# Kernel optimization log

Hardware: AMD Instinct MI355X
Metric: run time of the kernel (lower is better)

The kernel has to match this reference:

```python
import jax, jax.numpy as jnp
import numpy as np

INPUT_SIZE = 1
HIDDEN = 50
OUTPUT = 1
BATCH = 2048
SEQ = 512


def _lstm_layer(x, W_ih, W_hh, b_ih, b_hh):
    # x: [B, T, I]; W_ih: [4H, I]; W_hh: [4H, H]; biases: [4H]
    B = x.shape[0]
    H = W_hh.shape[1]
    # Precompute input contributions for all timesteps: [B, T, 4H]
    xg = jnp.einsum('bti,gi->btg', x, W_ih) + b_ih + b_hh

    def step(carry, xg_t):
        h, c = carry                      # [B, H] each
        g = xg_t + h @ W_hh.T             # [B, 4H]
        i, f, gg, o = jnp.split(g, 4, axis=-1)  # PyTorch gate order i,f,g,o
        i = jax.nn.sigmoid(i)
        f = jax.nn.sigmoid(f)
        gg = jnp.tanh(gg)
        o = jax.nn.sigmoid(o)
        c = f * c + i * gg
        h = o * jnp.tanh(c)
        return (h, c), h

    h0 = jnp.zeros((B, H), x.dtype)
    c0 = jnp.zeros((B, H), x.dtype)
    _, hs = jax.lax.scan(step, (h0, c0), jnp.swapaxes(xg, 0, 1))  # hs: [T, B, H]
    return jnp.swapaxes(hs, 0, 1)  # [B, T, H]


def setup_inputs() -> dict:
    key = jax.random.key(0)
    ks = jax.random.split(key, 11)
    s = 1.0 / np.sqrt(HIDDEN)  # PyTorch LSTM init scale
    x = jax.random.normal(ks[0], (BATCH, SEQ, INPUT_SIZE), dtype=jnp.float32)
    W_ih0 = jax.random.uniform(ks[1], (4 * HIDDEN, INPUT_SIZE), minval=-s, maxval=s)
    W_hh0 = jax.random.uniform(ks[2], (4 * HIDDEN, HIDDEN), minval=-s, maxval=s)
    b_ih0 = jax.random.uniform(ks[3], (4 * HIDDEN,), minval=-s, maxval=s)
    b_hh0 = jax.random.uniform(ks[4], (4 * HIDDEN,), minval=-s, maxval=s)
    W_ih1 = jax.random.uniform(ks[5], (4 * HIDDEN, HIDDEN), minval=-s, maxval=s)
    W_hh1 = jax.random.uniform(ks[6], (4 * HIDDEN, HIDDEN), minval=-s, maxval=s)
    b_ih1 = jax.random.uniform(ks[7], (4 * HIDDEN,), minval=-s, maxval=s)
    b_hh1 = jax.random.uniform(ks[8], (4 * HIDDEN,), minval=-s, maxval=s)
    fc_W = jax.random.uniform(ks[9], (OUTPUT, HIDDEN), minval=-s, maxval=s)
    fc_b = jax.random.uniform(ks[10], (OUTPUT,), minval=-s, maxval=s)
    return {
        'x': x,
        'W_ih0': W_ih0, 'W_hh0': W_hh0, 'b_ih0': b_ih0, 'b_hh0': b_hh0,
        'W_ih1': W_ih1, 'W_hh1': W_hh1, 'b_ih1': b_ih1, 'b_hh1': b_hh1,
        'fc_W': fc_W, 'fc_b': fc_b,
    }


def reference(x, W_ih0, W_hh0, b_ih0, b_hh0, W_ih1, W_hh1, b_ih1, b_hh1, fc_W, fc_b):
    h1 = _lstm_layer(x, W_ih0, W_hh0, b_ih0, b_hh0)   # [B, T, H]
    h2 = _lstm_layer(h1, W_ih1, W_hh1, b_ih1, b_hh1)  # [B, T, H]
    last = h2[:, -1, :]                               # [B, H]
    return last @ fc_W.T + fc_b                       # [B, OUTPUT]
```

## Files before the change

### kernel.cpp

```cpp
#include <hip/hip_runtime.h>

typedef _Float16 f16x8 __attribute__((ext_vector_type(8)));
typedef float    f32x4 __attribute__((ext_vector_type(4)));

constexpr int BATCH = 2048;
constexpr int SEQ   = 512;
constexpr int H     = 50;
constexpr int NB    = 8;
constexpr int NT    = 832;
constexpr int KQ    = 4;
constexpr int PSZ   = 1024;

__device__ __forceinline__ float fexp2(float x) { return __builtin_amdgcn_exp2f(x); }
__device__ __forceinline__ float frcp(float x)  { return __builtin_amdgcn_rcpf(x); }
__device__ __forceinline__ _Float16 f16hi(float w) { return (_Float16)w; }
__device__ __forceinline__ _Float16 f16lo(float w) {
    _Float16 h = (_Float16)w; return (_Float16)(w - (float)h);
}
__device__ __forceinline__ int caddr(int k, int c) {
    return ((k >> 3) * 64) + c * 8 + (k & 7);
}
union H2U { unsigned u; _Float16 h[2]; };

constexpr float K1 = 1.4426950408889634f;
constexpr float K2 = 2.8853900817779268f;


__global__ __launch_bounds__(NT, 3) void lstm2_r17(
    const float* __restrict__ x,
    const float* __restrict__ Wih0, const float* __restrict__ Whh0,
    const float* __restrict__ bih0, const float* __restrict__ bhh0,
    const float* __restrict__ Wih1, const float* __restrict__ Whh1,
    const float* __restrict__ bih1, const float* __restrict__ bhh1,
    const float* __restrict__ fcW,  const float* __restrict__ fcb,
    float* __restrict__ out)
{
    __shared__ _Float16 sB[2][PSZ];
    __shared__ unsigned sXu[SEQ * NB];
    __shared__ float    sH2f[H * NB];

    const int t    = threadIdx.x;
    const int wave = t >> 6, lane = t & 63;
    const int quad = lane >> 4, nn = lane & 15;
    const int bbase = blockIdx.x * NB;

    for (int i = t; i < 2 * PSZ; i += NT) ((_Float16*)sB)[i] = (_Float16)0.f;

    for (int i = t; i < NB * SEQ; i += NT) {
        const int b = i >> 9, s = i & (SEQ - 1);
        const float xv = x[(bbase + b) * SEQ + s];
        H2U p; p.h[0] = f16hi(xv); p.h[1] = f16lo(xv);
        sXu[s * NB + b] = p.u;
    }

    const int  m    = wave;
    const int  jr   = m * 4 + (nn >> 2);
    const int  gate = nn & 3;
    const bool rv   = (jr < H);
    const int  lrow = gate * H + jr;
    const float rsc = (gate == 2) ? -K2 : -K1;

    f16x8 a0[2];
    f16x8 a1[KQ];
    #pragma unroll
    for (int q = 0; q < 2; ++q) {
        #pragma unroll
        for (int j = 0; j < 8; ++j) {
            const int k = q * 32 + quad * 8 + j;
            _Float16 v = (_Float16)0.f;
            if (rv) {
                if      (k < 50)   v = (_Float16)(rsc * Whh0[lrow * H + k]);
                else if (k == 50)  v = f16hi(rsc * Wih0[lrow]);
                else if (k == 51)  v = f16lo(rsc * Wih0[lrow]);
            }
            a0[q][j] = v;
        }
    }
    #pragma unroll
    for (int q = 0; q < KQ; ++q) {
        #pragma unroll
        for (int j = 0; j < 8; ++j) {
            const int k = q * 32 + quad * 8 + j;
            _Float16 v = (_Float16)0.f;
            if (rv) {
                if      (k < 50)              v = (_Float16)(rsc * Wih1[lrow * H + k]);
                else if (k >= 64 && k < 114)  v = (_Float16)(rsc * Whh1[lrow * H + (k - 64)]);
            }
            a1[q][j] = v;
        }
    }

    const int  hiH  = nn >> 3;
    const int  col  = nn & 7;
    const int  jj   = m * 4 + quad;
    const bool jv   = (jj < H);

    f32x4 b0v = {0,0,0,0}, b1v = {0,0,0,0};
    if (jv) {
        #pragma unroll
        for (int r = 0; r < 4; ++r) {
            const float s = (r == 2) ? -K2 : -K1;
            b0v[r] = s * (bih0[r * H + jj] + bhh0[r * H + jj]);
            b1v[r] = s * (bih1[r * H + jj] + bhh1[r * H + jj]);
        }
    }

    const int rb0 = 0 * 256 + quad * 64 + col * 8;
    const int rb1 = 1 * 256 + quad * 64 + col * 8;
    const int rb2 = 2 * 256 + quad * 64 + col * 8;
    const int rb3 = 3 * 256 + quad * 64 + col * 8;
    const int  wH   = caddr(hiH * 64 + jj, col);
    const bool wrOK = jv;
    float c = 0.f;

    const bool xstage = (wave == 12) && (quad == 2) && (hiH == 0);
    const int  xwr    = (384 + col * 8 + 2) >> 1;

    __syncthreads();
    if (t < NB)
        ((unsigned*)sB[0])[(384 + t * 8 + 2) >> 1] = sXu[t];
    __syncthreads();

    auto body = [&](int s, const _Float16* __restrict__ br,
                    _Float16* __restrict__ bw,
                    bool doL0, bool doL1, bool last) {
        const f16x8 bq0 = *(const f16x8*)&br[rb0];
        const f16x8 bq1 = *(const f16x8*)&br[rb1];
        const f16x8 bq2 = *(const f16x8*)&br[rb2];
        const f16x8 bq3 = *(const f16x8*)&br[rb3];

        f32x4 g0 = b0v;
        g0 = __builtin_amdgcn_mfma_f32_16x16x32_f16(a0[0], bq0, g0, 0, 0, 0);
        g0 = __builtin_amdgcn_mfma_f32_16x16x32_f16(a0[1], bq1, g0, 0, 0, 0);
        f32x4 g1a = b1v;
        g1a = __builtin_amdgcn_mfma_f32_16x16x32_f16(a1[0], bq0, g1a, 0, 0, 0);
        g1a = __builtin_amdgcn_mfma_f32_16x16x32_f16(a1[1], bq1, g1a, 0, 0, 0);
        f32x4 g1b = {0, 0, 0, 0};
        g1b = __builtin_amdgcn_mfma_f32_16x16x32_f16(a1[2], bq2, g1b, 0, 0, 0);
        g1b = __builtin_amdgcn_mfma_f32_16x16x32_f16(a1[3], bq3, g1b, 0, 0, 0);

        float g[4];
        #pragma unroll
        for (int r = 0; r < 4; ++r)
            g[r] = hiH ? (g1a[r] + g1b[r]) : g0[r];

        const bool act = hiH ? doL1 : doL0;
        if (act) {
            float Ei = fexp2(g[0]);
            float Ef = fexp2(g[1]);
            float Eg = fexp2(-fabsf(g[2]));
            float Eo = fexp2(g[3]);
            float P  = (1.f + Ei) * (1.f + Eg);
            float F  = 1.f + Ef;
            float R  = frcp(P * F);
            float tn = copysignf((1.f - Eg) * F, -g[2]);
            c = fmaf(c, P, tn) * R;
            float Ec = fexp2(-fabsf(K2 * c));
            float h  = copysignf((1.f - Ec) * frcp((1.f + Eo) * (1.f + Ec)), c);
            if (wrOK) {
                if (last && hiH) {
                    sH2f[jj * NB + col] = h;
                } else {
                    bw[wH] = (_Float16)h;
                }
            }
        }
        if (xstage)
            ((unsigned*)bw)[xwr] = sXu[((s + 1) & (SEQ - 1)) * NB + col];
        __syncthreads();
    };

    body(0, sB[0], sB[1], true, false, false);
    #pragma unroll 1
    for (int i = 0; i < 255; ++i) {
        body(2 * i + 1, sB[1], sB[0], true, true, false);
        body(2 * i + 2, sB[0], sB[1], true, true, false);
    }
    body(511, sB[1], sB[0], true, true, false);
    body(512, sB[0], sB[1], false, true, true);

    if (t < NB) {
        float sum = fcb[0];
        #pragma unroll
        for (int jx = 0; jx < H; ++jx) sum += fcW[jx] * sH2f[jx * NB + t];
        out[bbase + t] = sum;
    }
}

extern "C" void kernel_launch(void* const* d_in, const int* in_sizes, int n_in,
                              void* d_out, int out_size, void* d_ws, size_t ws_size,
                              hipStream_t stream)
{
    const float* x    = (const float*)d_in[0];
    const float* Wih0 = (const float*)d_in[1];
    const float* Whh0 = (const float*)d_in[2];
    const float* bih0 = (const float*)d_in[3];
    const float* bhh0 = (const float*)d_in[4];
    const float* Wih1 = (const float*)d_in[5];
    const float* Whh1 = (const float*)d_in[6];
    const float* bih1 = (const float*)d_in[7];
    const float* bhh1 = (const float*)d_in[8];
    const float* fcW  = (const float*)d_in[9];
    const float* fcb  = (const float*)d_in[10];

    lstm2_r17<<<BATCH / NB, NT, 0, stream>>>(
        x, Wih0, Whh0, bih0, bhh0, Wih1, Whh1, bih1, bhh1, fcW, fcb,
        (float*)d_out);
}
```

Measured before the change: 319.9 us.

## Split LSTM layers into producer/consumer waves with LDS counter sync

```diff
diff --git a/kernel.cpp b/kernel.cpp
--- a/kernel.cpp
+++ b/kernel.cpp
@@ -7,9 +7,9 @@
 constexpr int SEQ   = 512;
 constexpr int H     = 50;
 constexpr int NB    = 8;
-constexpr int NT    = 832;
-constexpr int KQ    = 4;
-constexpr int PSZ   = 1024;
+constexpr int NT    = 896;
+constexpr int D     = 4;
+constexpr int PP    = 512;
 
 __device__ __forceinline__ float fexp2(float x) { return __builtin_amdgcn_exp2f(x); }
 __device__ __forceinline__ float frcp(float x)  { return __builtin_amdgcn_rcpf(x); }
@@ -26,7 +26,7 @@
 constexpr float K2 = 2.8853900817779268f;
 
 
-__global__ __launch_bounds__(NT, 3) void lstm2_r17(
+__global__ __launch_bounds__(NT, 4) void lstm2_pc(
     const float* __restrict__ x,
     const float* __restrict__ Wih0, const float* __restrict__ Whh0,
     const float* __restrict__ bih0, const float* __restrict__ bhh0,
@@ -35,150 +35,195 @@
     const float* __restrict__ fcW,  const float* __restrict__ fcb,
     float* __restrict__ out)
 {
-    __shared__ _Float16 sB[2][PSZ];
+    __shared__ _Float16 sRing[D][PP];
+    __shared__ _Float16 sH2[2][PP];
     __shared__ unsigned sXu[SEQ * NB];
     __shared__ float    sH2f[H * NB];
+    __shared__ unsigned sCnt[2];
 
     const int t    = threadIdx.x;
     const int wave = t >> 6, lane = t & 63;
     const int quad = lane >> 4, nn = lane & 15;
     const int bbase = blockIdx.x * NB;
 
-    for (int i = t; i < 2 * PSZ; i += NT) ((_Float16*)sB)[i] = (_Float16)0.f;
-
+    for (int i = t; i < D * PP; i += NT) ((_Float16*)sRing)[i] = (_Float16)0.f;
+    for (int i = t; i < 2 * PP; i += NT) ((_Float16*)sH2)[i]  = (_Float16)0.f;
+    if (t < 2) sCnt[t] = 0;
     for (int i = t; i < NB * SEQ; i += NT) {
         const int b = i >> 9, s = i & (SEQ - 1);
         const float xv = x[(bbase + b) * SEQ + s];
         H2U p; p.h[0] = f16hi(xv); p.h[1] = f16lo(xv);
         sXu[s * NB + b] = p.u;
     }
-
-    const int  m    = wave;
-    const int  jr   = m * 4 + (nn >> 2);
-    const int  gate = nn & 3;
-    const bool rv   = (jr < H);
-    const int  lrow = gate * H + jr;
-    const float rsc = (gate == 2) ? -K2 : -K1;
-
-    f16x8 a0[2];
-    f16x8 a1[KQ];
-    #pragma unroll
-    for (int q = 0; q < 2; ++q) {
-        #pragma unroll
-        for (int j = 0; j < 8; ++j) {
-            const int k = q * 32 + quad * 8 + j;
-            _Float16 v = (_Float16)0.f;
-            if (rv) {
-                if      (k < 50)   v = (_Float16)(rsc * Whh0[lrow * H + k]);
-                else if (k == 50)  v = f16hi(rsc * Wih0[lrow]);
-                else if (k == 51)  v = f16lo(rsc * Wih0[lrow]);
-            }
-            a0[q][j] = v;
-        }
-    }
-    #pragma unroll
-    for (int q = 0; q < KQ; ++q) {
-        #pragma unroll
-        for (int j = 0; j < 8; ++j) {
-            const int k = q * 32 + quad * 8 + j;
-            _Float16 v = (_Float16)0.f;
-            if (rv) {
-                if      (k < 50)              v = (_Float16)(rsc * Wih1[lrow * H + k]);
-                else if (k >= 64 && k < 114)  v = (_Float16)(rsc * Whh1[lrow * H + (k - 64)]);
-            }
-            a1[q][j] = v;
-        }
-    }
-
-    const int  hiH  = nn >> 3;
-    const int  col  = nn & 7;
-    const int  jj   = m * 4 + quad;
-    const bool jv   = (jj < H);
-
-    f32x4 b0v = {0,0,0,0}, b1v = {0,0,0,0};
-    if (jv) {
-        #pragma unroll
-        for (int r = 0; r < 4; ++r) {
-            const float s = (r == 2) ? -K2 : -K1;
-            b0v[r] = s * (bih0[r * H + jj] + bhh0[r * H + jj]);
-            b1v[r] = s * (bih1[r * H + jj] + bhh1[r * H + jj]);
-        }
-    }
-
-    const int rb0 = 0 * 256 + quad * 64 + col * 8;
-    const int rb1 = 1 * 256 + quad * 64 + col * 8;
-    const int rb2 = 2 * 256 + quad * 64 + col * 8;
-    const int rb3 = 3 * 256 + quad * 64 + col * 8;
-    const int  wH   = caddr(hiH * 64 + jj, col);
-    const bool wrOK = jv;
-    float c = 0.f;
-
-    const bool xstage = (wave == 12) && (quad == 2) && (hiH == 0);
-    const int  xwr    = (384 + col * 8 + 2) >> 1;
-
     __syncthreads();
     if (t < NB)
-        ((unsigned*)sB[0])[(384 + t * 8 + 2) >> 1] = sXu[t];
+        ((unsigned*)sRing[D - 1])[193 + 4 * t] = sXu[t];
     __syncthreads();
 
-    auto body = [&](int s, const _Float16* __restrict__ br,
-                    _Float16* __restrict__ bw,
-                    bool doL0, bool doL1, bool last) {
-        const f16x8 bq0 = *(const f16x8*)&br[rb0];
-        const f16x8 bq1 = *(const f16x8*)&br[rb1];
-        const f16x8 bq2 = *(const f16x8*)&br[rb2];
-        const f16x8 bq3 = *(const f16x8*)&br[rb3];
-
-        f32x4 g0 = b0v;
-        g0 = __builtin_amdgcn_mfma_f32_16x16x32_f16(a0[0], bq0, g0, 0, 0, 0);
-        g0 = __builtin_amdgcn_mfma_f32_16x16x32_f16(a0[1], bq1, g0, 0, 0, 0);
-        f32x4 g1a = b1v;
-        g1a = __builtin_amdgcn_mfma_f32_16x16x32_f16(a1[0], bq0, g1a, 0, 0, 0);
-        g1a = __builtin_amdgcn_mfma_f32_16x16x32_f16(a1[1], bq1, g1a, 0, 0, 0);
-        f32x4 g1b = {0, 0, 0, 0};
-        g1b = __builtin_amdgcn_mfma_f32_16x16x32_f16(a1[2], bq2, g1b, 0, 0, 0);
-        g1b = __builtin_amdgcn_mfma_f32_16x16x32_f16(a1[3], bq3, g1b, 0, 0, 0);
-
-        float g[4];
-        #pragma unroll
-        for (int r = 0; r < 4; ++r)
-            g[r] = hiH ? (g1a[r] + g1b[r]) : g0[r];
-
-        const bool act = hiH ? doL1 : doL0;
-        if (act) {
-            float Ei = fexp2(g[0]);
-            float Ef = fexp2(g[1]);
-            float Eg = fexp2(-fabsf(g[2]));
-            float Eo = fexp2(g[3]);
-            float P  = (1.f + Ei) * (1.f + Eg);
-            float F  = 1.f + Ef;
-            float R  = frcp(P * F);
-            float tn = copysignf((1.f - Eg) * F, -g[2]);
-            c = fmaf(c, P, tn) * R;
-            float Ec = fexp2(-fabsf(K2 * c));
-            float h  = copysignf((1.f - Ec) * frcp((1.f + Eo) * (1.f + Ec)), c);
-            if (wrOK) {
-                if (last && hiH) {
-                    sH2f[jj * NB + col] = h;
-                } else {
-                    bw[wH] = (_Float16)h;
+    const bool isL1 = (wave >= 7);
+    const int  wv   = isL1 ? wave - 7 : wave;
+    const int  T0   = wv, T1 = wv + 7;
+    const int  selT = nn >> 3;
+    const int  col  = nn & 7;
+    const int  jjS  = (selT ? T1 : T0) * 4 + quad;
+    const bool vOK  = (jjS < H);
+
+    volatile unsigned* vc0 = &sCnt[0];
+    volatile unsigned* vc1 = &sCnt[1];
+    auto waitge = [](volatile unsigned* c, unsigned tgt) {
+        while (*c < tgt) {}
+        __builtin_amdgcn_sched_barrier(0);
+        asm volatile("" ::: "memory");
+    };
+
+    f32x4 biasA = {0,0,0,0}, biasB = {0,0,0,0};
+    {
+        const float* bi = isL1 ? bih1 : bih0;
+        const float* bh = isL1 ? bhh1 : bhh0;
+        #pragma unroll
+        for (int r = 0; r < 4; ++r) {
+            const float sc = (r == 2) ? -K2 : -K1;
+            const int jqA = T0 * 4 + quad, jqB = T1 * 4 + quad;
+            biasA[r] = (jqA < H) ? sc * (bi[r * H + jqA] + bh[r * H + jqA]) : 0.f;
+            biasB[r] = (jqB < H) ? sc * (bi[r * H + jqB] + bh[r * H + jqB]) : 0.f;
+        }
+    }
+
+    const int rbase = quad * 64 + col * 8;
+    const int wslot = caddr(jjS < H ? jjS : 0, col);
+
+    if (!isL1) {
+        f16x8 aA[2][2];
+        #pragma unroll
+        for (int tt = 0; tt < 2; ++tt) {
+            const int  m    = tt ? T1 : T0;
+            const int  jr   = m * 4 + (nn >> 2);
+            const int  gate = nn & 3;
+            const bool rv   = (jr < H);
+            const int  lrow = gate * H + jr;
+            const float rsc = (gate == 2) ? -K2 : -K1;
+            #pragma unroll
+            for (int q = 0; q < 2; ++q) {
+                #pragma unroll
+                for (int j = 0; j < 8; ++j) {
+                    const int k = q * 32 + quad * 8 + j;
+                    _Float16 v = (_Float16)0.f;
+                    if (rv) {
+                        if      (k < 50)  v = (_Float16)(rsc * Whh0[lrow * H + k]);
+                        else if (k == 50) v = f16hi(rsc * Wih0[lrow]);
+                        else if (k == 51) v = f16lo(rsc * Wih0[lrow]);
+                    }
+                    aA[tt][q][j] = v;
                 }
             }
         }
-        if (xstage)
-            ((unsigned*)bw)[xwr] = sXu[((s + 1) & (SEQ - 1)) * NB + col];
-        __syncthreads();
-    };
-
-    body(0, sB[0], sB[1], true, false, false);
-    #pragma unroll 1
-    for (int i = 0; i < 255; ++i) {
-        body(2 * i + 1, sB[1], sB[0], true, true, false);
-        body(2 * i + 2, sB[0], sB[1], true, true, false);
-    }
-    body(511, sB[1], sB[0], true, true, false);
-    body(512, sB[0], sB[1], false, true, true);
-
+        const bool xst = (wv == 6) && (quad == 0) && (selT == 1);
+        float c = 0.f;
+        #pragma unroll 1
+        for (int s = 0; s < SEQ; ++s) {
+            waitge(vc0, 7u * (unsigned)s);
+            if (s >= D) waitge(vc1, 7u * (unsigned)(s - D + 1));
+            const _Float16* br = sRing[(s + D - 1) & (D - 1)];
+            _Float16*       bw = sRing[s & (D - 1)];
+            const f16x8 q0 = *(const f16x8*)&br[rbase];
+            const f16x8 q1 = *(const f16x8*)&br[256 + rbase];
+            f32x4 gA = biasA;
+            gA = __builtin_amdgcn_mfma_f32_16x16x32_f16(aA[0][0], q0, gA, 0, 0, 0);
+            gA = __builtin_amdgcn_mfma_f32_16x16x32_f16(aA[0][1], q1, gA, 0, 0, 0);
+            f32x4 gB = biasB;
+            gB = __builtin_amdgcn_mfma_f32_16x16x32_f16(aA[1][0], q0, gB, 0, 0, 0);
+            gB = __builtin_amdgcn_mfma_f32_16x16x32_f16(aA[1][1], q1, gB, 0, 0, 0);
+            float g[4];
+            #pragma unroll
+            for (int r = 0; r < 4; ++r) g[r] = selT ? gB[r] : gA[r];
+            {
+                float Ei = fexp2(g[0]);
+                float Ef = fexp2(g[1]);
+                float Eg = fexp2(-fabsf(g[2]));
+                float Eo = fexp2(g[3]);
+                float P  = (1.f + Ei) * (1.f + Eg);
+                float F  = 1.f + Ef;
+                float R  = frcp(P * F);
+                float tn = copysignf((1.f - Eg) * F, -g[2]);
+                c = fmaf(c, P, tn) * R;
+                float Ec = fexp2(-fabsf(K2 * c));
+                float h  = copysignf((1.f - Ec) * frcp((1.f + Eo) * (1.f + Ec)), c);
+                if (vOK) bw[wslot] = (_Float16)h;
+            }
+            if (xst) ((unsigned*)bw)[193 + 4 * col] = sXu[((s + 1) & (SEQ - 1)) * NB + col];
+            asm volatile("s_waitcnt lgkmcnt(0)" ::: "memory");
+            if (lane == 0) atomicAdd(&sCnt[0], 1u);
+        }
+    } else {
+        f16x8 aI[2][2], aH[2][2];
+        #pragma unroll
+        for (int tt = 0; tt < 2; ++tt) {
+            const int  m    = tt ? T1 : T0;
+            const int  jr   = m * 4 + (nn >> 2);
+            const int  gate = nn & 3;
+            const bool rv   = (jr < H);
+            const int  lrow = gate * H + jr;
+            const float rsc = (gate == 2) ? -K2 : -K1;
+            #pragma unroll
+            for (int q = 0; q < 2; ++q) {
+                #pragma unroll
+                for (int j = 0; j < 8; ++j) {
+                    const int k = q * 32 + quad * 8 + j;
+                    const bool kv = rv && (k < 50);
+                    aI[tt][q][j] = kv ? (_Float16)(rsc * Wih1[lrow * H + k]) : (_Float16)0.f;
+                    aH[tt][q][j] = kv ? (_Float16)(rsc * Whh1[lrow * H + k]) : (_Float16)0.f;
+                }
+            }
+        }
+        float c = 0.f;
+        #pragma unroll 1
+        for (int p = 0; p < SEQ; ++p) {
+            waitge(vc1, 7u * (unsigned)p);
+            waitge(vc0, 7u * (unsigned)(p + 1));
+            const _Float16* br = sRing[p & (D - 1)];
+            const _Float16* hr = sH2[p & 1];
+            _Float16*       hw = sH2[(p + 1) & 1];
+            const f16x8 q0 = *(const f16x8*)&br[rbase];
+            const f16x8 q1 = *(const f16x8*)&br[256 + rbase];
+            const f16x8 r0 = *(const f16x8*)&hr[rbase];
+            const f16x8 r1 = *(const f16x8*)&hr[256 + rbase];
+            f32x4 gAa = biasA, gBa = biasB;
+            gAa = __builtin_amdgcn_mfma_f32_16x16x32_f16(aI[0][0], q0, gAa, 0, 0, 0);
+            gAa = __builtin_amdgcn_mfma_f32_16x16x32_f16(aI[0][1], q1, gAa, 0, 0, 0);
+            gBa = __builtin_amdgcn_mfma_f32_16x16x32_f16(aI[1][0], q0, gBa, 0, 0, 0);
+            gBa = __builtin_amdgcn_mfma_f32_16x16x32_f16(aI[1][1], q1, gBa, 0, 0, 0);
+            f32x4 gAb = {0,0,0,0}, gBb = {0,0,0,0};
+            gAb = __builtin_amdgcn_mfma_f32_16x16x32_f16(aH[0][0], r0, gAb, 0, 0, 0);
+            gAb = __builtin_amdgcn_mfma_f32_16x16x32_f16(aH[0][1], r1, gAb, 0, 0, 0);
+            gBb = __builtin_amdgcn_mfma_f32_16x16x32_f16(aH[1][0], r0, gBb, 0, 0, 0);
+            gBb = __builtin_amdgcn_mfma_f32_16x16x32_f16(aH[1][1], r1, gBb, 0, 0, 0);
+            float g[4];
+            #pragma unroll
+            for (int r = 0; r < 4; ++r)
+                g[r] = selT ? (gBa[r] + gBb[r]) : (gAa[r] + gAb[r]);
+            {
+                float Ei = fexp2(g[0]);
+                float Ef = fexp2(g[1]);
+                float Eg = fexp2(-fabsf(g[2]));
+                float Eo = fexp2(g[3]);
+                float P  = (1.f + Ei) * (1.f + Eg);
+                float F  = 1.f + Ef;
+                float R  = frcp(P * F);
+                float tn = copysignf((1.f - Eg) * F, -g[2]);
+                c = fmaf(c, P, tn) * R;
+                float Ec = fexp2(-fabsf(K2 * c));
+                float h  = copysignf((1.f - Ec) * frcp((1.f + Eo) * (1.f + Ec)), c);
+                if (vOK) {
+                    if (p == SEQ - 1) sH2f[jjS * NB + col] = h;
+                    else              hw[wslot] = (_Float16)h;
+                }
+            }
+            asm volatile("s_waitcnt lgkmcnt(0)" ::: "memory");
+            if (lane == 0) atomicAdd(&sCnt[1], 1u);
+        }
+    }
+
+    __syncthreads();
     if (t < NB) {
         float sum = fcb[0];
         #pragma unroll
@@ -203,7 +248,7 @@
     const float* fcW  = (const float*)d_in[9];
     const float* fcb  = (const float*)d_in[10];
 
-    lstm2_r17<<<BATCH / NB, NT, 0, stream>>>(
+    lstm2_pc<<<BATCH / NB, NT, 0, stream>>>(
         x, Wih0, Whh0, bih0, bhh0, Wih1, Whh1, bih1, bhh1, fcW, fcb,
         (float*)d_out);
 }
```

Result: slower. 388.3 us (+21.4%).

## Split layer-0 and layer-1 work across separate wave groups

Applied to the files above, without the earlier changes.

```diff
diff --git a/kernel.cpp b/kernel.cpp
--- a/kernel.cpp
+++ b/kernel.cpp
@@ -7,8 +7,7 @@
 constexpr int SEQ   = 512;
 constexpr int H     = 50;
 constexpr int NB    = 8;
-constexpr int NT    = 832;
-constexpr int KQ    = 4;
+constexpr int NT    = 896;
 constexpr int PSZ   = 1024;
 
 __device__ __forceinline__ float fexp2(float x) { return __builtin_amdgcn_exp2f(x); }
@@ -26,7 +25,7 @@
 constexpr float K2 = 2.8853900817779268f;
 
 
-__global__ __launch_bounds__(NT, 3) void lstm2_r17(
+__global__ __launch_bounds__(NT, 3) void lstm2_rs(
     const float* __restrict__ x,
     const float* __restrict__ Wih0, const float* __restrict__ Whh0,
     const float* __restrict__ bih0, const float* __restrict__ bhh0,
@@ -53,120 +52,131 @@
         sXu[s * NB + b] = p.u;
     }
 
-    const int  m    = wave;
-    const int  jr   = m * 4 + (nn >> 2);
-    const int  gate = nn & 3;
-    const bool rv   = (jr < H);
-    const int  lrow = gate * H + jr;
-    const float rsc = (gate == 2) ? -K2 : -K1;
-
-    f16x8 a0[2];
-    f16x8 a1[KQ];
+    const bool isL1 = (wave >= 7);
+    const int  wv   = isL1 ? wave - 7 : wave;
+    const int  T0   = (wv < 6) ? 2 * wv     : 12;
+    const int  T1   = (wv < 6) ? 2 * wv + 1 : 13;
+    const int  selT = nn >> 3;
+    const int  col  = nn & 7;
+    const int  jjS  = (selT ? T1 : T0) * 4 + quad;
+    const bool vOK  = (jjS < H);
+
+    f16x8 aA[2][2];
+    f16x8 aI[2][2], aH[2][2];
     #pragma unroll
-    for (int q = 0; q < 2; ++q) {
+    for (int tt = 0; tt < 2; ++tt) {
+        const int  m    = tt ? T1 : T0;
+        const int  jr   = m * 4 + (nn >> 2);
+        const int  gate = nn & 3;
+        const bool rv   = (jr < H);
+        const int  lrow = gate * H + jr;
+        const float rsc = (gate == 2) ? -K2 : -K1;
         #pragma unroll
-        for (int j = 0; j < 8; ++j) {
-            const int k = q * 32 + quad * 8 + j;
-            _Float16 v = (_Float16)0.f;
-            if (rv) {
-                if      (k < 50)   v = (_Float16)(rsc * Whh0[lrow * H + k]);
-                else if (k == 50)  v = f16hi(rsc * Wih0[lrow]);
-                else if (k == 51)  v = f16lo(rsc * Wih0[lrow]);
+        for (int q = 0; q < 2; ++q) {
+            #pragma unroll
+            for (int j = 0; j < 8; ++j) {
+                const int k = q * 32 + quad * 8 + j;
+                _Float16 vA = (_Float16)0.f, vI = (_Float16)0.f, vH = (_Float16)0.f;
+                if (rv) {
+                    if (!isL1) {
+                        if      (k < 50)  vA = (_Float16)(rsc * Whh0[lrow * H + k]);
+                        else if (k == 50) vA = f16hi(rsc * Wih0[lrow]);
+                        else if (k == 51) vA = f16lo(rsc * Wih0[lrow]);
+                    } else if (k < 50) {
+                        vI = (_Float16)(rsc * Wih1[lrow * H + k]);
+                        vH = (_Float16)(rsc * Whh1[lrow * H + k]);
+                    }
+                }
+                aA[tt][q][j] = vA; aI[tt][q][j] = vI; aH[tt][q][j] = vH;
             }
-            a0[q][j] = v;
         }
     }
-    #pragma unroll
-    for (int q = 0; q < KQ; ++q) {
-        #pragma unroll
-        for (int j = 0; j < 8; ++j) {
-            const int k = q * 32 + quad * 8 + j;
-            _Float16 v = (_Float16)0.f;
-            if (rv) {
-                if      (k < 50)              v = (_Float16)(rsc * Wih1[lrow * H + k]);
-                else if (k >= 64 && k < 114)  v = (_Float16)(rsc * Whh1[lrow * H + (k - 64)]);
-            }
-            a1[q][j] = v;
-        }
-    }
-
-    const int  hiH  = nn >> 3;
-    const int  col  = nn & 7;
-    const int  jj   = m * 4 + quad;
-    const bool jv   = (jj < H);
-
-    f32x4 b0v = {0,0,0,0}, b1v = {0,0,0,0};
-    if (jv) {
+    f32x4 biasA = {0,0,0,0}, biasB = {0,0,0,0};
+    {
+        const float* bi = isL1 ? bih1 : bih0;
+        const float* bh = isL1 ? bhh1 : bhh0;
+        const int jqA = T0 * 4 + quad, jqB = T1 * 4 + quad;
         #pragma unroll
         for (int r = 0; r < 4; ++r) {
-            const float s = (r == 2) ? -K2 : -K1;
-            b0v[r] = s * (bih0[r * H + jj] + bhh0[r * H + jj]);
-            b1v[r] = s * (bih1[r * H + jj] + bhh1[r * H + jj]);
+            const float sc = (r == 2) ? -K2 : -K1;
+            biasA[r] = (jqA < H) ? sc * (bi[r * H + jqA] + bh[r * H + jqA]) : 0.f;
+            biasB[r] = (jqB < H) ? sc * (bi[r * H + jqB] + bh[r * H + jqB]) : 0.f;
         }
     }
 
-    const int rb0 = 0 * 256 + quad * 64 + col * 8;
-    const int rb1 = 1 * 256 + quad * 64 + col * 8;
-    const int rb2 = 2 * 256 + quad * 64 + col * 8;
-    const int rb3 = 3 * 256 + quad * 64 + col * 8;
-    const int  wH   = caddr(hiH * 64 + jj, col);
-    const bool wrOK = jv;
+    const int rb0 = quad * 64 + col * 8;
+    const int rb1 = 256 + rb0, rb2 = 512 + rb0, rb3 = 768 + rb0;
+    const int wslot = caddr((isL1 ? 64 : 0) + (vOK ? jjS : 0), col);
+    const bool xst  = (!isL1) && (wv == 6) && (quad == 0) && (selT == 1);
     float c = 0.f;
-
-    const bool xstage = (wave == 12) && (quad == 2) && (hiH == 0);
-    const int  xwr    = (384 + col * 8 + 2) >> 1;
 
     __syncthreads();
     if (t < NB)
-        ((unsigned*)sB[0])[(384 + t * 8 + 2) >> 1] = sXu[t];
+        ((unsigned*)sB[0])[193 + 4 * t] = sXu[t];
     __syncthreads();
+
+    auto act = [&](float g0, float g1, float g2, float g3) -> float {
+        float Ei = fexp2(g0);
+        float Ef = fexp2(g1);
+        float Eg = fexp2(-fabsf(g2));
+        float Eo = fexp2(g3);
+        float P  = (1.f + Ei) * (1.f + Eg);
+        float F  = 1.f + Ef;
+        float R  = frcp(P * F);
+        float tn = copysignf((1.f - Eg) * F, -g2);
+        c = fmaf(c, P, tn) * R;
+        float Ec = fexp2(-fabsf(K2 * c));
+        return copysignf((1.f - Ec) * frcp((1.f + Eo) * (1.f + Ec)), c);
+    };
 
     auto body = [&](int s, const _Float16* __restrict__ br,
                     _Float16* __restrict__ bw,
                     bool doL0, bool doL1, bool last) {
-        const f16x8 bq0 = *(const f16x8*)&br[rb0];
-        const f16x8 bq1 = *(const f16x8*)&br[rb1];
-        const f16x8 bq2 = *(const f16x8*)&br[rb2];
-        const f16x8 bq3 = *(const f16x8*)&br[rb3];
-
-        f32x4 g0 = b0v;
-        g0 = __builtin_amdgcn_mfma_f32_16x16x32_f16(a0[0], bq0, g0, 0, 0, 0);
-        g0 = __builtin_amdgcn_mfma_f32_16x16x32_f16(a0[1], bq1, g0, 0, 0, 0);
-        f32x4 g1a = b1v;
-        g1a = __builtin_amdgcn_mfma_f32_16x16x32_f16(a1[0], bq0, g1a, 0, 0, 0);
-        g1a = __builtin_amdgcn_mfma_f32_16x16x32_f16(a1[1], bq1, g1a, 0, 0, 0);
-        f32x4 g1b = {0, 0, 0, 0};
-        g1b = __builtin_amdgcn_mfma_f32_16x16x32_f16(a1[2], bq2, g1b, 0, 0, 0);
-        g1b = __builtin_amdgcn_mfma_f32_16x16x32_f16(a1[3], bq3, g1b, 0, 0, 0);
-
-        float g[4];
-        #pragma unroll
-        for (int r = 0; r < 4; ++r)
-            g[r] = hiH ? (g1a[r] + g1b[r]) : g0[r];
-
-        const bool act = hiH ? doL1 : doL0;
-        if (act) {
-            float Ei = fexp2(g[0]);
-            float Ef = fexp2(g[1]);
-            float Eg = fexp2(-fabsf(g[2]));
-            float Eo = fexp2(g[3]);
-            float P  = (1.f + Ei) * (1.f + Eg);
-            float F  = 1.f + Ef;
-            float R  = frcp(P * F);
-            float tn = copysignf((1.f - Eg) * F, -g[2]);
-            c = fmaf(c, P, tn) * R;
-            float Ec = fexp2(-fabsf(K2 * c));
-            float h  = copysignf((1.f - Ec) * frcp((1.f + Eo) * (1.f + Ec)), c);
-            if (wrOK) {
-                if (last && hiH) {
-                    sH2f[jj * NB + col] = h;
-                } else {
-                    bw[wH] = (_Float16)h;
+        if (!isL1) {
+            if (doL0) {
+                const f16x8 q0 = *(const f16x8*)&br[rb0];
+                const f16x8 q1 = *(const f16x8*)&br[rb1];
+                f32x4 gA = biasA;
+                gA = __builtin_amdgcn_mfma_f32_16x16x32_f16(aA[0][0], q0, gA, 0, 0, 0);
+                gA = __builtin_amdgcn_mfma_f32_16x16x32_f16(aA[0][1], q1, gA, 0, 0, 0);
+                f32x4 gB = biasB;
+                gB = __builtin_amdgcn_mfma_f32_16x16x32_f16(aA[1][0], q0, gB, 0, 0, 0);
+                gB = __builtin_amdgcn_mfma_f32_16x16x32_f16(aA[1][1], q1, gB, 0, 0, 0);
+                float h = act(selT ? gB[0] : gA[0], selT ? gB[1] : gA[1],
+                              selT ? gB[2] : gA[2], selT ? gB[3] : gA[3]);
+                if (vOK) bw[wslot] = (_Float16)h;
+            }
+            if (xst)
+                ((unsigned*)bw)[193 + 4 * col] = sXu[((s + 1) & (SEQ - 1)) * NB + col];
+        } else {
+            if (doL1) {
+                const f16x8 q0 = *(const f16x8*)&br[rb0];
+                const f16x8 q1 = *(const f16x8*)&br[rb1];
+                const f16x8 q2 = *(const f16x8*)&br[rb2];
+                const f16x8 q3 = *(const f16x8*)&br[rb3];
+                f32x4 gAa = biasA;
+                gAa = __builtin_amdgcn_mfma_f32_16x16x32_f16(aI[0][0], q0, gAa, 0, 0, 0);
+                gAa = __builtin_amdgcn_mfma_f32_16x16x32_f16(aI[0][1], q1, gAa, 0, 0, 0);
+                f32x4 gAb = {0,0,0,0};
+                gAb = __builtin_amdgcn_mfma_f32_16x16x32_f16(aH[0][0], q2, gAb, 0, 0, 0);
+                gAb = __builtin_amdgcn_mfma_f32_16x16x32_f16(aH[0][1], q3, gAb, 0, 0, 0);
+                f32x4 gBa = biasB;
+                gBa = __builtin_amdgcn_mfma_f32_16x16x32_f16(aI[1][0], q0, gBa, 0, 0, 0);
+                gBa = __builtin_amdgcn_mfma_f32_16x16x32_f16(aI[1][1], q1, gBa, 0, 0, 0);
+                f32x4 gBb = {0,0,0,0};
+                gBb = __builtin_amdgcn_mfma_f32_16x16x32_f16(aH[1][0], q2, gBb, 0, 0, 0);
+                gBb = __builtin_amdgcn_mfma_f32_16x16x32_f16(aH[1][1], q3, gBb, 0, 0, 0);
+                float g[4];
+                #pragma unroll
+                for (int r = 0; r < 4; ++r)
+                    g[r] = selT ? (gBa[r] + gBb[r]) : (gAa[r] + gAb[r]);
+                float h = act(g[0], g[1], g[2], g[3]);
+                if (vOK) {
+                    if (last) sH2f[jjS * NB + col] = h;
+                    else      bw[wslot] = (_Float16)h;
                 }
             }
         }
-        if (xstage)
-            ((unsigned*)bw)[xwr] = sXu[((s + 1) & (SEQ - 1)) * NB + col];
         __syncthreads();
     };
 
@@ -203,7 +213,7 @@
     const float* fcW  = (const float*)d_in[9];
     const float* fcb  = (const float*)d_in[10];
 
-    lstm2_r17<<<BATCH / NB, NT, 0, stream>>>(
+    lstm2_rs<<<BATCH / NB, NT, 0, stream>>>(
         x, Wih0, Whh0, bih0, bhh0, Wih1, Whh1, bih1, bhh1, fcW, fcb,
         (float*)d_out);
 }
```

New measurement: 315.0 us (median of 2 runs). About the same (-1.5%).
